# Performance work log

Hardware: AMD Instinct MI355X
Metric: run time of the kernel (lower is better)

Reference implementation:

```python
import jax, jax.numpy as jnp
import numpy as np

N = 100000      # num nodes
M = 25000       # num hyperedges
E = 600000      # num incidences (node, hyperedge) pairs
D_IN, D_HID, D_OUT = 128, 128, 128


def setup_inputs() -> dict:
    key = jax.random.key(0)
    ks = jax.random.split(key, 9)
    s_in = 1.0 / np.sqrt(D_IN)
    s_hid = 1.0 / np.sqrt(D_HID)
    return {
        "x": jax.random.normal(ks[0], (N, D_IN), dtype=jnp.float32),
        "W1": jax.random.normal(ks[1], (D_IN, D_HID), dtype=jnp.float32) * s_in,
        "b1": jnp.zeros((D_HID,), dtype=jnp.float32),
        "W2": jax.random.normal(ks[2], (D_HID, D_HID), dtype=jnp.float32) * s_hid,
        "b2": jnp.zeros((D_HID,), dtype=jnp.float32),
        "W3": jax.random.normal(ks[3], (D_HID, D_OUT), dtype=jnp.float32) * s_hid,
        "b3": jnp.zeros((D_OUT,), dtype=jnp.float32),
        "node_idx": jax.random.randint(ks[4], (E,), 0, N, dtype=jnp.int32),
        "hedge_idx": jax.random.randint(ks[5], (E,), 0, M, dtype=jnp.int32),
        "num_hyperedges": M,
    }


def _hypergraph_conv(x, W, b, node_idx, hedge_idx, num_hyperedges):
    """PyG HypergraphConv (use_attention=False, hyperedge_weight=1):
    out = D^-1 H B^-1 H^T (x @ W) + b
    """
    n = x.shape[0]
    x = x @ W                                   # [N, F_out]
    ones = jnp.ones(node_idx.shape[0], dtype=x.dtype)
    deg_n = jax.ops.segment_sum(ones, node_idx, num_segments=n)              # D
    deg_e = jax.ops.segment_sum(ones, hedge_idx, num_segments=num_hyperedges)  # B
    d_inv = jnp.where(deg_n > 0, 1.0 / deg_n, 0.0)
    b_inv = jnp.where(deg_e > 0, 1.0 / deg_e, 0.0)
    # node -> hyperedge: m_e = B^-1 sum_{i in e} x_i
    m = jax.ops.segment_sum(x[node_idx], hedge_idx, num_segments=num_hyperedges)
    m = m * b_inv[:, None]
    # hyperedge -> node: out_i = D^-1 sum_{e ni i} m_e
    out = jax.ops.segment_sum(m[hedge_idx], node_idx, num_segments=n)
    out = out * d_inv[:, None]
    return out + b


def reference(x, W1, b1, W2, b2, W3, b3, node_idx, hedge_idx, num_hyperedges):
    # dropout is identity in eval mode (training=False)
    x = jax.nn.elu(_hypergraph_conv(x, W1, b1, node_idx, hedge_idx, num_hyperedges))
    x = jax.nn.elu(_hypergraph_conv(x, W2, b2, node_idx, hedge_idx, num_hyperedges))
    x = jax.nn.elu(_hypergraph_conv(x, W3, b3, node_idx, hedge_idx, num_hyperedges))
    return x
```

## Files before the change

kernel.cpp:

```cpp
#include <hip/hip_runtime.h>

#define NN 100000
#define MM 25000
#define EE 600000
#define TT (MM + NN)

#define CVT_BLOCKS 12500
#define NB 782
#define CAP 2048
#define TILE_E 4096
#define GA ((EE + TILE_E - 1) / TILE_E)

typedef __attribute__((ext_vector_type(8))) short short8;
typedef __attribute__((ext_vector_type(4))) float floatx4;

__device__ __forceinline__ float bl(unsigned int u){ return __uint_as_float(u << 16); }
__device__ __forceinline__ float bh(unsigned int u){ return __uint_as_float(u & 0xffff0000u); }
__device__ __forceinline__ unsigned int packbf2(float a, float b){
    unsigned int ua = __float_as_uint(a), ub = __float_as_uint(b);
    ua = (ua + 0x7fffu + ((ua >> 16) & 1u)) >> 16;
    ub = (ub + 0x7fffu + ((ub >> 16) & 1u)) & 0xffff0000u;
    return ua | ub;
}
__device__ __forceinline__ unsigned short f2bf(float f){
    unsigned int u = __float_as_uint(f);
    return (unsigned short)((u + 0x7fffu + ((u >> 16) & 1u)) >> 16);
}
__device__ __forceinline__ void acc8(float* a, uint4 v){
    a[0] += bl(v.x); a[1] += bh(v.x);
    a[2] += bl(v.y); a[3] += bh(v.y);
    a[4] += bl(v.z); a[5] += bh(v.z);
    a[6] += bl(v.w); a[7] += bh(v.w);
}

__global__ void k_setup(const float* __restrict__ x, unsigned int* __restrict__ xb,
                        const float* __restrict__ W1, const float* __restrict__ W2,
                        const float* __restrict__ W3, unsigned short* __restrict__ WT,
                        int* __restrict__ gcur) {
    int b = blockIdx.x;
    if (b < CVT_BLOCKS) {
        int t = b * 256 + threadIdx.x;
        float4 v = ((const float4*)x)[t];
        uint2 o; o.x = packbf2(v.x, v.y); o.y = packbf2(v.z, v.w);
        ((uint2*)xb)[t] = o;
    } else if (b < CVT_BLOCKS + 3) {
        int l = b - CVT_BLOCKS;
        const float* W = l == 0 ? W1 : (l == 1 ? W2 : W3);
        unsigned short* T = WT + l * 16384;
        for (int i = threadIdx.x; i < 16384; i += 256) {
            int k = i >> 7, c = i & 127;
            T[c * 128 + k] = f2bf(W[k * 128 + c]);
        }
    } else {
        for (int i = threadIdx.x; i < NB; i += 256) gcur[i] = i * CAP;
    }
}

__global__ __launch_bounds__(256) void k_binA(const int* __restrict__ nidx, const int* __restrict__ hidx,
                                              int* __restrict__ gcur, unsigned int* __restrict__ items) {
    __shared__ int h[NB];
    __shared__ int cur[NB];
    int t = threadIdx.x;
    for (int i = t; i < NB; i += 256) h[i] = 0;
    __syncthreads();
    int base = blockIdx.x * TILE_E;
    #pragma unroll
    for (int k = 0; k < 16; k++) {
        int e = base + k * 256 + t;
        if (e < EE) {
            atomicAdd(&h[hidx[e] >> 6], 1);
            atomicAdd(&h[391 + (nidx[e] >> 8)], 1);
        }
    }
    __syncthreads();
    for (int i = t; i < NB; i += 256) {
        int c = h[i];
        cur[i] = c ? atomicAdd(&gcur[i], c) : 0;
    }
    __syncthreads();
    #pragma unroll
    for (int k = 0; k < 16; k++) {
        int e = base + k * 256 + t;
        if (e < EE) {
            int hh = hidx[e], nn = nidx[e];
            int p1 = atomicAdd(&cur[hh >> 6], 1);
            items[p1] = ((unsigned)(hh & 63) << 17) | (unsigned)nn;
            int p2 = atomicAdd(&cur[391 + (nn >> 8)], 1);
            items[p2] = ((unsigned)(nn & 255) << 15) | (unsigned)hh;
        }
    }
}

__global__ __launch_bounds__(256) void k_passB(unsigned int* __restrict__ items,
                                               const int* __restrict__ gcur,
                                               int2* __restrict__ ptr2, float* __restrict__ inv) {
    __shared__ unsigned int led[CAP];
    __shared__ unsigned int grp[CAP];
    __shared__ int bins[256], cur[256], tmp[256];
    int b = blockIdx.x, t = threadIdx.x;
    int base = b * CAP, cnt = gcur[b] - base;
    bool he = b < 391;
    int nbins = he ? 64 : 256;
    int keybase = he ? b * 64 : MM + (b - 391) * 256;
    int shift = he ? 17 : 15;
    unsigned int mask = he ? 0x1FFFFu : 0x7FFFu;
    int keylim = he ? MM : TT;

    for (int i = t; i < cnt; i += 256) led[i] = items[base + i];
    bins[t] = 0;
    __syncthreads();
    for (int i = t; i < cnt; i += 256) atomicAdd(&bins[led[i] >> shift], 1);
    __syncthreads();
    int v = (t < nbins) ? bins[t] : 0;
    tmp[t] = v;
    __syncthreads();
    for (int o = 1; o < 256; o <<= 1) {
        int u = (t >= o) ? tmp[t - o] : 0;
        __syncthreads();
        tmp[t] += u;
        __syncthreads();
    }
    int excl = tmp[t] - v;
    if (t < nbins) {
        int g = keybase + t;
        if (g < keylim) {
            ptr2[g] = make_int2(base + excl, v);
            inv[g] = v ? 1.f / (float)v : 0.f;
        }
        cur[t] = excl;
    }
    __syncthreads();
    for (int i = t; i < cnt; i += 256) {
        unsigned int it = led[i];
        int p = atomicAdd(&cur[it >> shift], 1);
        grp[p] = it & mask;
    }
    __syncthreads();
    for (int i = t; i < cnt; i += 256) items[base + i] = grp[i];
}

__device__ __forceinline__ void gather_row8(const unsigned int* __restrict__ X,
                                            const unsigned int* __restrict__ adj,
                                            int beg, int deg, int ql, float* a) {
    int end = beg + deg;
    for (int j = beg; j < end; j += 8) {
        int c = end - j;
        int n[8];
        #pragma unroll
        for (int i = 0; i < 8; i++) n[i] = (i < c) ? (int)adj[j + i] : 0;
        uint4 z = make_uint4(0u, 0u, 0u, 0u);
        uint4 v[8];
        #pragma unroll
        for (int i = 0; i < 8; i++) {
            v[i] = z;
            if (i < c) v[i] = *((const uint4*)(X + (unsigned)n[i] * 64u) + ql);
        }
        #pragma unroll
        for (int i = 0; i < 8; i++) acc8(a, v[i]);
    }
}

__global__ __launch_bounds__(256) void k_hegemm(const unsigned int* __restrict__ X,
        const int2* __restrict__ ptr2, const unsigned int* __restrict__ adj,
        const float* __restrict__ b_inv, const unsigned short* __restrict__ WT,
        unsigned short* __restrict__ C) {
    __shared__ unsigned int tile[16 * 68];
    int t = threadIdx.x;
    int qidx = t >> 4, ql = t & 15;
    int r0 = blockIdx.x * 16;
    int r = r0 + qidx;
    float a[8] = {0.f,0.f,0.f,0.f,0.f,0.f,0.f,0.f};
    float sc = 0.f;
    if (r < MM) {
        int2 pe = ptr2[r];
        gather_row8(X, adj, pe.x, pe.y, ql, a);
        sc = b_inv[r];
    }
    uint4 o;
    o.x = packbf2(a[0] * sc, a[1] * sc);
    o.y = packbf2(a[2] * sc, a[3] * sc);
    o.z = packbf2(a[4] * sc, a[5] * sc);
    o.w = packbf2(a[6] * sc, a[7] * sc);
    *((uint4*)(tile + qidx * 68 + ql * 4)) = o;
    __syncthreads();

    int wv = t >> 6, lane = t & 63;
    int mm = lane & 15, quad = lane >> 4;
    floatx4 acc0 = (floatx4){0.f,0.f,0.f,0.f}, acc1 = acc0;
    int c0 = wv * 2;
    #pragma unroll
    for (int q = 0; q < 4; q++) {
        short8 af = *reinterpret_cast<const short8*>((const short*)(tile + mm * 68) + q * 32 + quad * 8);
        short8 b0 = *reinterpret_cast<const short8*>(WT + (c0 * 16 + mm) * 128 + q * 32 + quad * 8);
        short8 b1 = *reinterpret_cast<const short8*>(WT + ((c0 + 1) * 16 + mm) * 128 + q * 32 + quad * 8);
        acc0 = __builtin_amdgcn_mfma_f32_16x16x32_bf16(af, b0, acc0, 0, 0, 0);
        acc1 = __builtin_amdgcn_mfma_f32_16x16x32_bf16(af, b1, acc1, 0, 0, 0);
    }
    #pragma unroll
    for (int rg = 0; rg < 4; rg++) {
        int rr = r0 + quad * 4 + rg;
        if (rr < MM) {
            C[rr * 128 + c0 * 16 + mm]       = f2bf(acc0[rg]);
            C[rr * 128 + (c0 + 1) * 16 + mm] = f2bf(acc1[rg]);
        }
    }
}

template<bool F32OUT>
__global__ __launch_bounds__(256) void k_gather_nd(const unsigned int* __restrict__ X,
        const int2* __restrict__ ptr2, const unsigned int* __restrict__ adj,
        const float* __restrict__ d_inv, const float* __restrict__ bias, void* __restrict__ out) {
    int gw = (blockIdx.x * 256 + threadIdx.x) >> 6;
    int lane = threadIdx.x & 63, quad = lane >> 4, ql = lane & 15;
    int r = gw * 4 + quad;
    if (r >= NN) return;
    int2 pe = ptr2[r];
    float a[8] = {0.f,0.f,0.f,0.f,0.f,0.f,0.f,0.f};
    gather_row8(X, adj, pe.x, pe.y, ql, a);
    float sc = d_inv[r];
    const float4* b4 = (const float4*)bias;
    float4 bA = b4[ql * 2], bB = b4[ql * 2 + 1];
    float f[8];
    f[0] = a[0] * sc + bA.x; f[1] = a[1] * sc + bA.y;
    f[2] = a[2] * sc + bA.z; f[3] = a[3] * sc + bA.w;
    f[4] = a[4] * sc + bB.x; f[5] = a[5] * sc + bB.y;
    f[6] = a[6] * sc + bB.z; f[7] = a[7] * sc + bB.w;
    #pragma unroll
    for (int i = 0; i < 8; i++) f[i] = f[i] > 0.f ? f[i] : __expf(f[i]) - 1.f;
    if (F32OUT) {
        float* o = (float*)out + (unsigned)r * 128u;
        ((float4*)o)[ql * 2]     = make_float4(f[0], f[1], f[2], f[3]);
        ((float4*)o)[ql * 2 + 1] = make_float4(f[4], f[5], f[6], f[7]);
    } else {
        uint4 o4;
        o4.x = packbf2(f[0], f[1]); o4.y = packbf2(f[2], f[3]);
        o4.z = packbf2(f[4], f[5]); o4.w = packbf2(f[6], f[7]);
        ((uint4*)((unsigned int*)out + (unsigned)r * 64u))[ql] = o4;
    }
}

extern "C" void kernel_launch(void* const* d_in, const int* in_sizes, int n_in,
                              void* d_out, int out_size, void* d_ws, size_t ws_size,
                              hipStream_t stream) {
    const float* x  = (const float*)d_in[0];
    const float* W1 = (const float*)d_in[1];
    const float* b1 = (const float*)d_in[2];
    const float* W2 = (const float*)d_in[3];
    const float* b2 = (const float*)d_in[4];
    const float* W3 = (const float*)d_in[5];
    const float* b3 = (const float*)d_in[6];
    const int* nidx = (const int*)d_in[7];
    const int* hidx = (const int*)d_in[8];

    char* ws = (char*)d_ws;
    size_t o = 0;
    auto alloc = [&](size_t b) -> char* { char* p = ws + o; o = (o + b + 255) & ~(size_t)255; return p; };
    int2*  ptr2  = (int2*)alloc((size_t)TT * 8);
    float* invq  = (float*)alloc(TT * 4);
    int*   gcur  = (int*)alloc(NB * 4);
    unsigned int* items = (unsigned int*)alloc((size_t)NB * CAP * 4);
    unsigned short* WT   = (unsigned short*)alloc(3 * 128 * 128 * 2);
    unsigned short* mbuf = (unsigned short*)alloc((size_t)MM * 128 * 2);

    unsigned int* xb   = (unsigned int*)d_out;
    unsigned int* bufA = (unsigned int*)d_out;
    unsigned int* bufB = (unsigned int*)d_out + (size_t)NN * 64;

    k_setup<<<CVT_BLOCKS + 4, 256, 0, stream>>>(x, xb, W1, W2, W3, WT, gcur);
    k_binA<<<GA, 256, 0, stream>>>(nidx, hidx, gcur, items);
    k_passB<<<NB, 256, 0, stream>>>(items, gcur, ptr2, invq);

    const float* b_inv = invq;
    const float* d_inv = invq + MM;
    const int2* nptr2 = ptr2 + MM;
    const int grid_hg = (MM + 15) / 16;
    const int grid_nd = NN * 64 / 256;
    const unsigned int* adj = items;

    k_hegemm<<<grid_hg, 256, 0, stream>>>(xb, ptr2, adj, b_inv, WT, mbuf);
    k_gather_nd<false><<<grid_nd, 256, 0, stream>>>((const unsigned int*)mbuf, nptr2, adj, d_inv, b1, (void*)bufA);
    k_hegemm<<<grid_hg, 256, 0, stream>>>(bufA, ptr2, adj, b_inv, WT + 16384, mbuf);
    k_gather_nd<false><<<grid_nd, 256, 0, stream>>>((const unsigned int*)mbuf, nptr2, adj, d_inv, b2, (void*)bufB);
    k_hegemm<<<grid_hg, 256, 0, stream>>>(bufB, ptr2, adj, b_inv, WT + 32768, mbuf);
    k_gather_nd<true ><<<grid_nd, 256, 0, stream>>>((const unsigned int*)mbuf, nptr2, adj, d_inv, b3, d_out);
}
```

Before: 362.2 us.

## Split gather from GEMM and gather feature slices in column passes

Separates the hyperedge gather from the MFMA projection into two kernels, with a new intermediate buffer. Each gather now walks the adjacency list once per column slice, 4 passes of 64 bytes for hyperedges and 2 passes of 128 bytes for nodes, instead of loading the full 256-byte row at once. The node gather becomes grid-strided over 2048 blocks, so each pass across all rows sees a smaller working set of columns. The aim is better L2/cache locality on the random row gathers and a standalone GEMM that computes all 128 output columns per wave. The cost is an extra kernel launch and an extra round trip through memory for the intermediate per layer, plus re-reading the index lists once per pass.

```diff
diff --git a/kernel.cpp b/kernel.cpp
--- a/kernel.cpp
+++ b/kernel.cpp
@@ -10,6 +10,10 @@
 #define CAP 2048
 #define TILE_E 4096
 #define GA ((EE + TILE_E - 1) / TILE_E)
+
+#define GB_HE 1563
+#define NT_ND 6250
+#define GB_ND 2048
 
 typedef __attribute__((ext_vector_type(8))) short short8;
 typedef __attribute__((ext_vector_type(4))) float floatx4;
@@ -25,12 +29,6 @@
 __device__ __forceinline__ unsigned short f2bf(float f){
     unsigned int u = __float_as_uint(f);
     return (unsigned short)((u + 0x7fffu + ((u >> 16) & 1u)) >> 16);
-}
-__device__ __forceinline__ void acc8(float* a, uint4 v){
-    a[0] += bl(v.x); a[1] += bh(v.x);
-    a[2] += bl(v.y); a[3] += bh(v.y);
-    a[4] += bl(v.z); a[5] += bh(v.z);
-    a[6] += bl(v.w); a[7] += bh(v.w);
 }
 
 __global__ void k_setup(const float* __restrict__ x, unsigned int* __restrict__ xb,
@@ -139,103 +137,114 @@
     for (int i = t; i < cnt; i += 256) items[base + i] = grp[i];
 }
 
-__device__ __forceinline__ void gather_row8(const unsigned int* __restrict__ X,
-                                            const unsigned int* __restrict__ adj,
-                                            int beg, int deg, int ql, float* a) {
-    int end = beg + deg;
-    for (int j = beg; j < end; j += 8) {
-        int c = end - j;
-        int n[8];
-        #pragma unroll
-        for (int i = 0; i < 8; i++) n[i] = (i < c) ? (int)adj[j + i] : 0;
-        uint4 z = make_uint4(0u, 0u, 0u, 0u);
-        uint4 v[8];
-        #pragma unroll
-        for (int i = 0; i < 8; i++) {
-            v[i] = z;
-            if (i < c) v[i] = *((const uint4*)(X + (unsigned)n[i] * 64u) + ql);
-        }
-        #pragma unroll
-        for (int i = 0; i < 8; i++) acc8(a, v[i]);
-    }
-}
-
-__global__ __launch_bounds__(256) void k_hegemm(const unsigned int* __restrict__ X,
+__global__ __launch_bounds__(256) void k_gather_heq(const unsigned int* __restrict__ X,
         const int2* __restrict__ ptr2, const unsigned int* __restrict__ adj,
-        const float* __restrict__ b_inv, const unsigned short* __restrict__ WT,
-        unsigned short* __restrict__ C) {
-    __shared__ unsigned int tile[16 * 68];
+        const float* __restrict__ b_inv, unsigned int* __restrict__ sbuf) {
     int t = threadIdx.x;
     int qidx = t >> 4, ql = t & 15;
-    int r0 = blockIdx.x * 16;
-    int r = r0 + qidx;
-    float a[8] = {0.f,0.f,0.f,0.f,0.f,0.f,0.f,0.f};
-    float sc = 0.f;
-    if (r < MM) {
-        int2 pe = ptr2[r];
-        gather_row8(X, adj, pe.x, pe.y, ql, a);
-        sc = b_inv[r];
-    }
-    uint4 o;
-    o.x = packbf2(a[0] * sc, a[1] * sc);
-    o.y = packbf2(a[2] * sc, a[3] * sc);
-    o.z = packbf2(a[4] * sc, a[5] * sc);
-    o.w = packbf2(a[6] * sc, a[7] * sc);
-    *((uint4*)(tile + qidx * 68 + ql * 4)) = o;
-    __syncthreads();
-
-    int wv = t >> 6, lane = t & 63;
-    int mm = lane & 15, quad = lane >> 4;
-    floatx4 acc0 = (floatx4){0.f,0.f,0.f,0.f}, acc1 = acc0;
-    int c0 = wv * 2;
-    #pragma unroll
-    for (int q = 0; q < 4; q++) {
-        short8 af = *reinterpret_cast<const short8*>((const short*)(tile + mm * 68) + q * 32 + quad * 8);
-        short8 b0 = *reinterpret_cast<const short8*>(WT + (c0 * 16 + mm) * 128 + q * 32 + quad * 8);
-        short8 b1 = *reinterpret_cast<const short8*>(WT + ((c0 + 1) * 16 + mm) * 128 + q * 32 + quad * 8);
-        acc0 = __builtin_amdgcn_mfma_f32_16x16x32_bf16(af, b0, acc0, 0, 0, 0);
-        acc1 = __builtin_amdgcn_mfma_f32_16x16x32_bf16(af, b1, acc1, 0, 0, 0);
-    }
-    #pragma unroll
-    for (int rg = 0; rg < 4; rg++) {
-        int rr = r0 + quad * 4 + rg;
-        if (rr < MM) {
-            C[rr * 128 + c0 * 16 + mm]       = f2bf(acc0[rg]);
-            C[rr * 128 + (c0 + 1) * 16 + mm] = f2bf(acc1[rg]);
-        }
+    int r = blockIdx.x * 16 + qidx;
+    if (r >= MM) return;
+    int2 pe = ptr2[r];
+    float sc = b_inv[r];
+    int end = pe.x + pe.y;
+    #pragma unroll
+    for (int p = 0; p < 4; ++p) {
+        float a0 = 0.f, a1 = 0.f;
+        for (int j = pe.x; j < end; j += 8) {
+            int c = end - j;
+            int n[8];
+            #pragma unroll
+            for (int i = 0; i < 8; i++) n[i] = (i < c) ? (int)adj[j + i] : 0;
+            unsigned int v[8];
+            #pragma unroll
+            for (int i = 0; i < 8; i++) {
+                v[i] = 0u;
+                if (i < c) v[i] = X[(unsigned)n[i] * 64u + p * 16 + ql];
+            }
+            #pragma unroll
+            for (int i = 0; i < 8; i++) { a0 += bl(v[i]); a1 += bh(v[i]); }
+        }
+        sbuf[(unsigned)r * 64u + p * 16 + ql] = packbf2(a0 * sc, a1 * sc);
     }
 }
 
 template<bool F32OUT>
-__global__ __launch_bounds__(256) void k_gather_nd(const unsigned int* __restrict__ X,
+__global__ __launch_bounds__(256) void k_gather_ndh(const unsigned int* __restrict__ X,
         const int2* __restrict__ ptr2, const unsigned int* __restrict__ adj,
         const float* __restrict__ d_inv, const float* __restrict__ bias, void* __restrict__ out) {
-    int gw = (blockIdx.x * 256 + threadIdx.x) >> 6;
-    int lane = threadIdx.x & 63, quad = lane >> 4, ql = lane & 15;
-    int r = gw * 4 + quad;
-    if (r >= NN) return;
-    int2 pe = ptr2[r];
-    float a[8] = {0.f,0.f,0.f,0.f,0.f,0.f,0.f,0.f};
-    gather_row8(X, adj, pe.x, pe.y, ql, a);
-    float sc = d_inv[r];
-    const float4* b4 = (const float4*)bias;
-    float4 bA = b4[ql * 2], bB = b4[ql * 2 + 1];
-    float f[8];
-    f[0] = a[0] * sc + bA.x; f[1] = a[1] * sc + bA.y;
-    f[2] = a[2] * sc + bA.z; f[3] = a[3] * sc + bA.w;
-    f[4] = a[4] * sc + bB.x; f[5] = a[5] * sc + bB.y;
-    f[6] = a[6] * sc + bB.z; f[7] = a[7] * sc + bB.w;
-    #pragma unroll
-    for (int i = 0; i < 8; i++) f[i] = f[i] > 0.f ? f[i] : __expf(f[i]) - 1.f;
-    if (F32OUT) {
-        float* o = (float*)out + (unsigned)r * 128u;
-        ((float4*)o)[ql * 2]     = make_float4(f[0], f[1], f[2], f[3]);
-        ((float4*)o)[ql * 2 + 1] = make_float4(f[4], f[5], f[6], f[7]);
-    } else {
-        uint4 o4;
-        o4.x = packbf2(f[0], f[1]); o4.y = packbf2(f[2], f[3]);
-        o4.z = packbf2(f[4], f[5]); o4.w = packbf2(f[6], f[7]);
-        ((uint4*)((unsigned int*)out + (unsigned)r * 64u))[ql] = o4;
+    int t = threadIdx.x;
+    int qidx = t >> 4, ql = t & 15;
+    const uint2* X2 = (const uint2*)X;
+    #pragma unroll
+    for (int p = 0; p < 2; ++p) {
+        for (int tile = blockIdx.x; tile < NT_ND; tile += GB_ND) {
+            int r = tile * 16 + qidx;
+            if (r >= NN) continue;
+            int2 pe = ptr2[r];
+            int end = pe.x + pe.y;
+            float a0 = 0.f, a1 = 0.f, a2 = 0.f, a3 = 0.f;
+            for (int j = pe.x; j < end; j += 8) {
+                int c = end - j;
+                int n[8];
+                #pragma unroll
+                for (int i = 0; i < 8; i++) n[i] = (i < c) ? (int)adj[j + i] : 0;
+                uint2 v[8];
+                #pragma unroll
+                for (int i = 0; i < 8; i++) {
+                    v[i] = make_uint2(0u, 0u);
+                    if (i < c) v[i] = X2[(unsigned)n[i] * 32u + p * 16 + ql];
+                }
+                #pragma unroll
+                for (int i = 0; i < 8; i++) {
+                    a0 += bl(v[i].x); a1 += bh(v[i].x);
+                    a2 += bl(v[i].y); a3 += bh(v[i].y);
+                }
+            }
+            float sc = d_inv[r];
+            float4 bb = ((const float4*)bias)[p * 16 + ql];
+            float f0 = a0 * sc + bb.x, f1 = a1 * sc + bb.y;
+            float f2 = a2 * sc + bb.z, f3 = a3 * sc + bb.w;
+            f0 = f0 > 0.f ? f0 : __expf(f0) - 1.f;
+            f1 = f1 > 0.f ? f1 : __expf(f1) - 1.f;
+            f2 = f2 > 0.f ? f2 : __expf(f2) - 1.f;
+            f3 = f3 > 0.f ? f3 : __expf(f3) - 1.f;
+            if (F32OUT) {
+                ((float4*)out)[(unsigned)r * 32u + p * 16 + ql] = make_float4(f0, f1, f2, f3);
+            } else {
+                ((uint2*)out)[(unsigned)r * 32u + p * 16 + ql] = make_uint2(packbf2(f0, f1), packbf2(f2, f3));
+            }
+        }
+    }
+}
+
+__global__ __launch_bounds__(256) void k_gemm(const unsigned short* __restrict__ A,
+                                              const unsigned short* __restrict__ WT,
+                                              unsigned short* __restrict__ C) {
+    int lane = threadIdx.x & 63;
+    int wv = threadIdx.x >> 6;
+    int r0 = blockIdx.x * 64 + wv * 16;
+    int mm = lane & 15;
+    int quad = lane >> 4;
+    floatx4 acc[8];
+    #pragma unroll
+    for (int c = 0; c < 8; c++) acc[c] = (floatx4){0.f, 0.f, 0.f, 0.f};
+    int arow = r0 + mm; if (arow >= MM) arow = MM - 1;
+    #pragma unroll
+    for (int q = 0; q < 4; q++) {
+        short8 af = *reinterpret_cast<const short8*>(A + arow * 128 + q * 32 + quad * 8);
+        #pragma unroll
+        for (int c = 0; c < 8; c++) {
+            short8 bf = *reinterpret_cast<const short8*>(WT + (c * 16 + mm) * 128 + q * 32 + quad * 8);
+            acc[c] = __builtin_amdgcn_mfma_f32_16x16x32_bf16(af, bf, acc[c], 0, 0, 0);
+        }
+    }
+    #pragma unroll
+    for (int c = 0; c < 8; c++) {
+        #pragma unroll
+        for (int r = 0; r < 4; r++) {
+            int row = r0 + quad * 4 + r;
+            if (row < MM) C[row * 128 + c * 16 + mm] = f2bf(acc[c][r]);
+        }
     }
 }
 
@@ -260,6 +269,7 @@
     int*   gcur  = (int*)alloc(NB * 4);
     unsigned int* items = (unsigned int*)alloc((size_t)NB * CAP * 4);
     unsigned short* WT   = (unsigned short*)alloc(3 * 128 * 128 * 2);
+    unsigned short* sbuf = (unsigned short*)alloc((size_t)MM * 128 * 2);
     unsigned short* mbuf = (unsigned short*)alloc((size_t)MM * 128 * 2);
 
     unsigned int* xb   = (unsigned int*)d_out;
@@ -273,14 +283,16 @@
     const float* b_inv = invq;
     const float* d_inv = invq + MM;
     const int2* nptr2 = ptr2 + MM;
-    const int grid_hg = (MM + 15) / 16;
-    const int grid_nd = NN * 64 / 256;
     const unsigned int* adj = items;
-
-    k_hegemm<<<grid_hg, 256, 0, stream>>>(xb, ptr2, adj, b_inv, WT, mbuf);
-    k_gather_nd<false><<<grid_nd, 256, 0, stream>>>((const unsigned int*)mbuf, nptr2, adj, d_inv, b1, (void*)bufA);
-    k_hegemm<<<grid_hg, 256, 0, stream>>>(bufA, ptr2, adj, b_inv, WT + 16384, mbuf);
-    k_gather_nd<false><<<grid_nd, 256, 0, stream>>>((const unsigned int*)mbuf, nptr2, adj, d_inv, b2, (void*)bufB);
-    k_hegemm<<<grid_hg, 256, 0, stream>>>(bufB, ptr2, adj, b_inv, WT + 32768, mbuf);
-    k_gather_nd<true ><<<grid_nd, 256, 0, stream>>>((const unsigned int*)mbuf, nptr2, adj, d_inv, b3, d_out);
-}
+    const int grid_gm = (MM + 63) / 64;
+
+    k_gather_heq<<<GB_HE, 256, 0, stream>>>(xb, ptr2, adj, b_inv, (unsigned int*)sbuf);
+    k_gemm<<<grid_gm, 256, 0, stream>>>(sbuf, WT, mbuf);
+    k_gather_ndh<false><<<GB_ND, 256, 0, stream>>>((const unsigned int*)mbuf, nptr2, adj, d_inv, b1, (void*)bufA);
+    k_gather_heq<<<GB_HE, 256, 0, stream>>>(bufA, ptr2, adj, b_inv, (unsigned int*)sbuf);
+    k_gemm<<<grid_gm, 256, 0, stream>>>(sbuf, WT + 16384, mbuf);
+    k_gather_ndh<false><<<GB_ND, 256, 0, stream>>>((const unsigned int*)mbuf, nptr2, adj, d_inv, b2, (void*)bufB);
+    k_gather_heq<<<GB_HE, 256, 0, stream>>>(bufB, ptr2, adj, b_inv, (unsigned int*)sbuf);
+    k_gemm<<<grid_gm, 256, 0, stream>>>(sbuf, WT + 32768, mbuf);
+    k_gather_ndh<true ><<<GB_ND, 256, 0, stream>>>((const unsigned int*)mbuf, nptr2, adj, d_inv, b3, d_out);
+}
```

Result: slower. 477.9 us (+32.0%).
